# Optimization experiments

Measured on AMD Instinct MI355X. Metric: run time of the kernel, lower is better.

The kernel has to match this reference:

```python
import jax, jax.numpy as jnp
import numpy as np
from jax import lax

VTH = 0.5
GRAD_WIN = 0.5
CDECAY = 0.5
VDECAY = 0.75

@jax.custom_vjp
def pseudo_spike(v):
    # PseudoSpikeRect: heaviside fwd, rectangular surrogate grad bwd
    return (v > VTH).astype(v.dtype)

def _ps_fwd(v):
    return pseudo_spike(v), v

def _ps_bwd(v, g):
    return (g * (jnp.abs(v - VTH) < GRAD_WIN).astype(g.dtype),)

pseudo_spike.defvjp(_ps_fwd, _ps_bwd)

def conv2d(x, w, b):
    y = lax.conv_general_dilated(x, w, (1, 1), 'VALID',
                                 dimension_numbers=('NCHW', 'OIHW', 'NCHW'))
    return y + b[None, :, None, None]

def lif(psp, state):
    # CUBA-LIF: current decay + integrate, voltage decay with spike reset, threshold
    cur, volt, spk = state
    cur = CDECAY * cur + psp
    volt = VDECAY * volt * (1.0 - spk) + cur
    spk = pseudo_spike(volt)
    return spk, (cur, volt, spk)

def setup_inputs() -> dict:
    key = jax.random.key(0)
    ks = jax.random.split(key, 16)
    B, T = 64, 200
    c1, c2, c3 = 64, 128, 256
    s = lambda k, shape, scale: jax.random.normal(k, shape, jnp.float32) * scale
    return {
        'input_data': jax.random.normal(ks[0], (B, 1, 10, 10, T), jnp.float32),
        'conv1_w': s(ks[1], (c1, 1, 3, 3), 0.3), 'conv1_b': s(ks[2], (c1,), 0.1),
        'conv2_w': s(ks[3], (c2, c1, 3, 3), 0.05), 'conv2_b': s(ks[4], (c2,), 0.1),
        'conv3_w': s(ks[5], (c3, c2, 3, 3), 0.03), 'conv3_b': s(ks[6], (c3,), 0.1),
        'tc_w': s(ks[7], (3, c3, c3), 0.06), 'tc_b': s(ks[8], (3, c3), 0.1),
        'rec_w': s(ks[9], (c3, c3), 0.06), 'rec_b': s(ks[10], (c3,), 0.1),
        'fc1_w': s(ks[11], (128, c3), 0.06), 'fc1_b': s(ks[12], (128,), 0.1),
        'fc2_w': s(ks[13], (2, 128), 0.09),
        'ts_weights': jnp.ones((T, 1), jnp.float32) / T,
    }

def reference(input_data, conv1_w, conv1_b, conv2_w, conv2_b, conv3_w, conv3_b,
              tc_w, tc_b, rec_w, rec_b, fc1_w, fc1_b, fc2_w, ts_weights):
    B = input_data.shape[0]
    c1, c2, c3 = conv1_w.shape[0], conv2_w.shape[0], conv3_w.shape[0]
    f1 = fc1_w.shape[0]

    def zs(shape):
        z = jnp.zeros(shape, input_data.dtype)
        return (z, z, z)

    carry0 = (zs((B, c1, 8, 8)), zs((B, c2, 6, 6)), zs((B, c3, 1, 1)),
              zs((B, c3)), zs((B, c3)), zs((B, f1)),
              jnp.zeros((3, B, c3), input_data.dtype),  # temporal buffer, idx0 = newest
              jnp.int32(0))
    xs = jnp.moveaxis(input_data, -1, 0)  # [T, B, 1, 10, 10]

    def step_fn(carry, xw):
        c1_st, c2_st, c3_st, tc_st, r_st, f_st, buf, step = carry
        x, w = xw
        s1, c1_st = lif(conv2d(x, conv1_w, conv1_b), c1_st)       # [B,c1,8,8]
        s2, c2_st = lif(conv2d(s1, conv2_w, conv2_b), c2_st)      # [B,c2,6,6]
        p = s2.reshape(B, c2, 3, 2, 3, 2).mean(axis=(3, 5))       # AvgPool2d(2) -> [B,c2,3,3]
        s3, c3_st = lif(conv2d(p, conv3_w, conv3_b), c3_st)       # [B,c3,1,1]
        flat = s3.reshape(B, -1)                                   # [B,c3]
        buf = jnp.concatenate([flat[None], buf[:2]], axis=0)
        # temporal conv: tap i applies to spike at time t-i, only if it exists
        psp = jnp.zeros_like(flat)
        for i in range(3):
            tap = buf[i] @ tc_w[i].T + tc_b[i]
            psp = psp + jnp.where(step >= i, 1.0, 0.0).astype(tap.dtype) * tap
        s_tc, tc_st = lif(psp, tc_st)
        # recurrent cell: identity feedforward + linear on previous spike
        psp_r = s_tc + r_st[2] @ rec_w.T + rec_b
        s_r, r_st = lif(psp_r, r_st)
        s_f, f_st = lif(s_r @ fc1_w.T + fc1_b, f_st)
        out = (s_f @ fc2_w.T) * w  # w = ts_weights[step], shape [1]
        return (c1_st, c2_st, c3_st, tc_st, r_st, f_st, buf, step + 1), out

    _, outs = lax.scan(step_fn, carry0, (xs, ts_weights))
    return outs.sum(axis=0)  # [B, 2]
```

## Files before the change

kernel.cpp:

```cpp
#include <hip/hip_runtime.h>


#define B_   64
#define T_   200
#define TCB_ 50

__device__ __forceinline__ void lif32(float psp, float& cur, float& volt, float& spk) {
#pragma clang fp contract(off)
    cur  = __fadd_rn(__fmul_rn(0.5f, cur), psp);
    volt = __fadd_rn(__fmul_rn(__fmul_rn(0.75f, volt), __fsub_rn(1.0f, spk)), cur);
    spk  = (volt > 0.5f) ? 1.0f : 0.0f;
}

__global__ void k_setup(const float* __restrict__ w2, const float* __restrict__ w3,
                        const float* __restrict__ tcw, const float* __restrict__ recw,
                        const float* __restrict__ fw,
                        float* __restrict__ w2T, float* __restrict__ w3T,
                        float* __restrict__ tcT, float* __restrict__ recT,
                        float* __restrict__ fc1T) {
    int idx = blockIdx.x * 256 + threadIdx.x;
    if (idx < 73728) { int o = idx & 127, k = idx >> 7; w2T[idx] = w2[o * 576 + k]; return; }
    idx -= 73728;
    if (idx < 294912) { int o = idx & 255, k = idx >> 8; w3T[idx] = w3[o * 1152 + k]; return; }
    idx -= 294912;
    if (idx < 196608) { int tap = idx >> 16, r = idx & 65535; int o = r & 255, k = r >> 8;
                        tcT[idx] = tcw[tap * 65536 + o * 256 + k]; return; }
    idx -= 196608;
    if (idx < 65536) { int o = idx & 255, k = idx >> 8; recT[idx] = recw[o * 256 + k]; return; }
    idx -= 65536;
    if (idx < 32768) { int o = idx & 127, k = idx >> 7; fc1T[idx] = fw[o * 256 + k]; return; }
}

__global__ __launch_bounds__(256) void k_conv1(const float* __restrict__ x,
                                               const float* __restrict__ w1,
                                               const float* __restrict__ b1,
                                               unsigned char* __restrict__ s1c,
                                               float* __restrict__ st1,
                                               int t0, int TC, int first) {
    int idx = blockIdx.x * 256 + threadIdx.x;
    int xx = idx & 7, yy = (idx >> 3) & 7, o = (idx >> 6) & 63, b = idx >> 12;
    float w[9];
#pragma unroll
    for (int i = 0; i < 9; i++) w[i] = w1[o * 9 + i];
    float bias = b1[o];
    const float* xb = x + (size_t)b * 20000;
    unsigned char* sb = s1c + (size_t)b * TC * 4096 + (o << 6) + (yy << 3) + xx;
    float cur, volt, spk;
    if (first) { cur = 0.f; volt = 0.f; spk = 0.f; }
    else { cur = st1[idx]; volt = st1[262144 + idx]; spk = st1[524288 + idx]; }
    for (int tl = 0; tl < TC; tl += 4) {
        int t = t0 + tl;
        float a0 = 0.f, a1 = 0.f, a2 = 0.f, a3 = 0.f;
#pragma unroll
        for (int i = 0; i < 3; i++) {
#pragma unroll
            for (int j = 0; j < 3; j++) {
                float4 v = *(const float4*)&xb[((yy + i) * 10 + xx + j) * T_ + t];
                float wv = w[i * 3 + j];
                a0 = fmaf(wv, v.x, a0); a1 = fmaf(wv, v.y, a1);
                a2 = fmaf(wv, v.z, a2); a3 = fmaf(wv, v.w, a3);
            }
        }
        float accs[4] = {a0, a1, a2, a3};
#pragma unroll
        for (int q = 0; q < 4; q++) {
            float psp = __fadd_rn(accs[q], bias);
            lif32(psp, cur, volt, spk);
            sb[(size_t)(tl + q) * 4096] = (unsigned char)spk;
        }
    }
    st1[idx] = cur; st1[262144 + idx] = volt; st1[524288 + idx] = spk;
}

__global__ __launch_bounds__(192) void k_conv2(const unsigned char* __restrict__ s1c,
                                               const float* __restrict__ w2T,
                                               const float* __restrict__ b2,
                                               float* __restrict__ psp2c) {
    __shared__ float a_s[4096];
    int blk = blockIdx.x;
    int tid = threadIdx.x;
    const unsigned int* src4 = (const unsigned int*)(s1c + (size_t)blk * 4096);
    for (int i = tid; i < 1024; i += 192) {
        unsigned int u = src4[i];
        a_s[4 * i + 0] = (float)(u & 0xff);
        a_s[4 * i + 1] = (float)((u >> 8) & 0xff);
        a_s[4 * i + 2] = (float)((u >> 16) & 0xff);
        a_s[4 * i + 3] = (float)(u >> 24);
    }
    __syncthreads();
    int quad = tid / 6;
    int y = tid - quad * 6;
    int ob = quad << 2;
    float acc[4][6];
#pragma unroll
    for (int oo = 0; oo < 4; oo++)
#pragma unroll
        for (int xq = 0; xq < 6; xq++) acc[oo][xq] = 0.f;
    for (int c = 0; c < 64; c++) {
#pragma unroll
        for (int i = 0; i < 3; i++) {
            const float* ar = &a_s[c * 64 + (y + i) * 8];
            float4 f0 = *(const float4*)(ar);
            float4 f1 = *(const float4*)(ar + 4);
            float a[8] = {f0.x, f0.y, f0.z, f0.w, f1.x, f1.y, f1.z, f1.w};
            const float* wr = w2T + (size_t)((c * 3 + i) * 3) * 128 + ob;
#pragma unroll
            for (int j = 0; j < 3; j++) {
                float4 wv = *(const float4*)(wr + j * 128);
                float w4[4] = {wv.x, wv.y, wv.z, wv.w};
#pragma unroll
                for (int oo = 0; oo < 4; oo++)
#pragma unroll
                    for (int xq = 0; xq < 6; xq++)
                        acc[oo][xq] = fmaf(w4[oo], a[xq + j], acc[oo][xq]);
            }
        }
    }
    size_t obase = (size_t)blk * 4608 + (size_t)ob * 36 + y * 6;
#pragma unroll
    for (int oo = 0; oo < 4; oo++) {
        float bv = b2[ob + oo];
        float* dst = psp2c + obase + oo * 36;
#pragma unroll
        for (int xq = 0; xq < 6; xq++)
            dst[xq] = __fadd_rn(acc[oo][xq], bv);
    }
}

__global__ __launch_bounds__(256) void k_lif2pool(const float* __restrict__ psp2c,
                                                  float* __restrict__ pc,
                                                  float* __restrict__ st2,
                                                  int TC, int first) {
    int idx = blockIdx.x * 256 + threadIdx.x;
    int px = idx % 3; int r = idx / 3; int py = r % 3; r /= 3;
    int o = r & 127, b = r >> 7;
    const float* pb = psp2c + (size_t)b * TC * 4608 + o * 36;
    float* pd = pc + (size_t)b * TC * 1152 + o * 9 + py * 3 + px;
    int off0 = (2 * py) * 6 + 2 * px, off1 = off0 + 6;
    float c0, c1, c2, c3, v0, v1, v2, v3, s0, s1, s2, s3;
    if (first) {
        c0 = c1 = c2 = c3 = v0 = v1 = v2 = v3 = s0 = s1 = s2 = s3 = 0.f;
    } else {
        c0 = st2[idx];              c1 = st2[73728 + idx];
        c2 = st2[147456 + idx];     c3 = st2[221184 + idx];
        v0 = st2[294912 + idx];     v1 = st2[368640 + idx];
        v2 = st2[442368 + idx];     v3 = st2[516096 + idx];
        s0 = st2[589824 + idx];     s1 = st2[663552 + idx];
        s2 = st2[737280 + idx];     s3 = st2[811008 + idx];
    }
    for (int tl = 0; tl < TC; tl++) {
        const float* pt = pb + (size_t)tl * 4608;
        float2 ra = *(const float2*)(pt + off0);
        float2 rb = *(const float2*)(pt + off1);
        lif32(ra.x, c0, v0, s0);
        lif32(ra.y, c1, v1, s1);
        lif32(rb.x, c2, v2, s2);
        lif32(rb.y, c3, v3, s3);
        pd[(size_t)tl * 1152] = __fmul_rn(0.25f, __fadd_rn(__fadd_rn(__fadd_rn(s0, s1), s2), s3));
    }
    st2[idx] = c0;           st2[73728 + idx] = c1;
    st2[147456 + idx] = c2;  st2[221184 + idx] = c3;
    st2[294912 + idx] = v0;  st2[368640 + idx] = v1;
    st2[442368 + idx] = v2;  st2[516096 + idx] = v3;
    st2[589824 + idx] = s0;  st2[663552 + idx] = s1;
    st2[737280 + idx] = s2;  st2[811008 + idx] = s3;
}

__global__ __launch_bounds__(256) void k_conv3(const float* __restrict__ pc,
                                               const float* __restrict__ w3T,
                                               const float* __restrict__ b3,
                                               float* __restrict__ psp3c) {
    __shared__ float a_s[16 * 288];
    int row0 = blockIdx.x * 16;
    int tid = threadIdx.x;
    int oq = tid & 63, mg = tid >> 6;
    float acc[4][4];
#pragma unroll
    for (int oo = 0; oo < 4; oo++)
#pragma unroll
        for (int mi = 0; mi < 4; mi++) acc[oo][mi] = 0.f;
    for (int kc = 0; kc < 1152; kc += 288) {
        __syncthreads();
        for (int idx = tid; idx < 16 * 288; idx += 256) {
            int m = idx / 288, k = idx - m * 288;
            a_s[idx] = pc[(size_t)(row0 + m) * 1152 + kc + k];
        }
        __syncthreads();
        for (int k = 0; k < 288; k++) {
            float4 wv = *(const float4*)&w3T[(size_t)(kc + k) * 256 + (oq << 2)];
            float w4[4] = {wv.x, wv.y, wv.z, wv.w};
            float am[4];
#pragma unroll
            for (int mi = 0; mi < 4; mi++) am[mi] = a_s[(mg * 4 + mi) * 288 + k];
#pragma unroll
            for (int oo = 0; oo < 4; oo++)
#pragma unroll
                for (int mi = 0; mi < 4; mi++)
                    acc[oo][mi] = fmaf(w4[oo], am[mi], acc[oo][mi]);
        }
    }
#pragma unroll
    for (int mi = 0; mi < 4; mi++) {
        float* dst = psp3c + (size_t)(row0 + mg * 4 + mi) * 256 + (oq << 2);
#pragma unroll
        for (int oo = 0; oo < 4; oo++)
            dst[oo] = __fadd_rn(acc[oo][mi], b3[(oq << 2) + oo]);
    }
}

__global__ __launch_bounds__(256) void k_scan3(const float* __restrict__ psp3c,
                                               unsigned char* __restrict__ s3u8,
                                               float* __restrict__ st3,
                                               int t0, int TC, int first) {
    int idx = blockIdx.x * 256 + threadIdx.x;
    int b = idx >> 8, n = idx & 255;
    float cur, volt, spk;
    if (first) { cur = 0.f; volt = 0.f; spk = 0.f; }
    else { cur = st3[idx]; volt = st3[16384 + idx]; spk = st3[32768 + idx]; }
    for (int tl = 0; tl < TC; tl++) {
        lif32(psp3c[(size_t)(b * TC + tl) * 256 + n], cur, volt, spk);
        s3u8[((size_t)b * T_ + t0 + tl) * 256 + n] = (unsigned char)spk;
    }
    st3[idx] = cur; st3[16384 + idx] = volt; st3[32768 + idx] = spk;
}

__global__ __launch_bounds__(256) void k_tc(const unsigned char* __restrict__ s3u8,
                                            const float* __restrict__ tcT,
                                            const float* __restrict__ tc_b,
                                            float* __restrict__ ptcc, int t0) {
    __shared__ float a_s[16 * 256];
    int crow0 = blockIdx.x * 16;
    int tid = threadIdx.x;
    int oq = tid & 63, mg = tid >> 6;
    float psum[4][4];
#pragma unroll
    for (int oo = 0; oo < 4; oo++)
#pragma unroll
        for (int mi = 0; mi < 4; mi++) psum[oo][mi] = 0.f;
    for (int tap = 0; tap < 3; tap++) {
        __syncthreads();
        for (int idx = tid; idx < 16 * 256; idx += 256) {
            int m = idx >> 8, k = idx & 255;
            int crow = crow0 + m;
            int b = crow / TCB_, tl = crow - b * TCB_;
            int t = t0 + tl;
            float v = 0.f;
            if (t >= tap) v = (float)s3u8[((size_t)b * T_ + t - tap) * 256 + k];
            a_s[idx] = v;
        }
        __syncthreads();
        float acc[4][4];
#pragma unroll
        for (int oo = 0; oo < 4; oo++)
#pragma unroll
            for (int mi = 0; mi < 4; mi++) acc[oo][mi] = 0.f;
        const float* wbase = tcT + (size_t)tap * 65536 + (oq << 2);
        for (int k = 0; k < 256; k++) {
            float4 wv = *(const float4*)(wbase + (size_t)k * 256);
            float w4[4] = {wv.x, wv.y, wv.z, wv.w};
            float am[4];
#pragma unroll
            for (int mi = 0; mi < 4; mi++) am[mi] = a_s[(mg * 4 + mi) * 256 + k];
#pragma unroll
            for (int oo = 0; oo < 4; oo++)
#pragma unroll
                for (int mi = 0; mi < 4; mi++)
                    acc[oo][mi] = fmaf(w4[oo], am[mi], acc[oo][mi]);
        }
#pragma unroll
        for (int mi = 0; mi < 4; mi++) {
            int crow = crow0 + mg * 4 + mi;
            int b = crow / TCB_, tl = crow - b * TCB_;
            int t = t0 + tl;
            float g = (t >= tap) ? 1.0f : 0.0f;
#pragma unroll
            for (int oo = 0; oo < 4; oo++) {
                int oc = (oq << 2) + oo;
                float tap_f = __fadd_rn(acc[oo][mi], tc_b[tap * 256 + oc]);
                psum[oo][mi] = __fadd_rn(psum[oo][mi], __fmul_rn(g, tap_f));
            }
        }
    }
#pragma unroll
    for (int mi = 0; mi < 4; mi++) {
        int crow = crow0 + mg * 4 + mi;
        float* dst = ptcc + (size_t)crow * 256 + (oq << 2);
#pragma unroll
        for (int oo = 0; oo < 4; oo++) dst[oo] = psum[oo][mi];
    }
}

__global__ __launch_bounds__(256) void k_scan_tc(const float* __restrict__ ptcc,
                                                 unsigned char* __restrict__ s_tc8,
                                                 float* __restrict__ st_tc,
                                                 int t0, int first) {
    int idx = blockIdx.x * 256 + threadIdx.x;
    int b = idx >> 8, n = idx & 255;
    float cur, volt, spk;
    if (first) { cur = 0.f; volt = 0.f; spk = 0.f; }
    else { cur = st_tc[idx]; volt = st_tc[16384 + idx]; spk = st_tc[32768 + idx]; }
    for (int tl = 0; tl < TCB_; tl++) {
        lif32(ptcc[(size_t)(b * TCB_ + tl) * 256 + n], cur, volt, spk);
        s_tc8[((size_t)b * T_ + t0 + tl) * 256 + n] = (unsigned char)spk;
    }
    st_tc[idx] = cur; st_tc[16384 + idx] = volt; st_tc[32768 + idx] = spk;
}

__global__ __launch_bounds__(512, 1) void k_rec(const unsigned char* __restrict__ s_tc8,
                                                const float* __restrict__ rec_w,
                                                const float* __restrict__ rec_b,
                                                unsigned char* __restrict__ s_r8) {
    __shared__ __align__(16) float spk_s[2][256];
    __shared__ float acc_s[256];
    int b = blockIdx.x;
    int tid = threadIdx.x;
    int o = tid & 255, half = tid >> 8;
    float w[128];
#pragma unroll
    for (int j = 0; j < 32; j++) {
        float4 v = *(const float4*)&rec_w[(size_t)o * 256 + (half << 7) + 4 * j];
        w[4 * j + 0] = v.x; w[4 * j + 1] = v.y;
        w[4 * j + 2] = v.z; w[4 * j + 3] = v.w;
    }
#pragma unroll
    for (int k = 0; k < 128; k++) asm volatile("" : "+v"(w[k]));
    if (half == 0) spk_s[0][o] = 0.f;
    float cur = 0.f, volt = 0.f, spk = 0.f;
    float rb = rec_b[o];
    const unsigned char* stp = s_tc8 + (size_t)b * T_ * 256 + o;
    unsigned char* srp = s_r8 + (size_t)b * T_ * 256 + o;
    __syncthreads();
    int p = 0;
    for (int t = 0; t < T_; t++) {
        if (half == 0) {
            const float* sp = spk_s[p];
            float acc = 0.f;
#pragma unroll
            for (int k = 0; k < 128; k += 4) {
                float4 sv = *(const float4*)&sp[k];
                acc = fmaf(sv.x, w[k + 0], acc);
                acc = fmaf(sv.y, w[k + 1], acc);
                acc = fmaf(sv.z, w[k + 2], acc);
                acc = fmaf(sv.w, w[k + 3], acc);
            }
            acc_s[o] = acc;
        }
        __syncthreads();
        if (half == 1) {
            float stc = (float)stp[(size_t)t * 256];
            const float* sp = spk_s[p] + 128;
            float acc = acc_s[o];
#pragma unroll
            for (int k = 0; k < 128; k += 4) {
                float4 sv = *(const float4*)&sp[k];
                acc = fmaf(sv.x, w[k + 0], acc);
                acc = fmaf(sv.y, w[k + 1], acc);
                acc = fmaf(sv.z, w[k + 2], acc);
                acc = fmaf(sv.w, w[k + 3], acc);
            }
            float psp = __fadd_rn(__fadd_rn(stc, acc), rb);
            lif32(psp, cur, volt, spk);
            srp[(size_t)t * 256] = (unsigned char)spk;
            spk_s[p ^ 1][o] = spk;
        }
        __syncthreads();
        p ^= 1;
    }
}

__global__ __launch_bounds__(256) void k_fc1(const unsigned char* __restrict__ s_r8,
                                             const float* __restrict__ fc1T,
                                             const float* __restrict__ fc1_b,
                                             float* __restrict__ pfc, int t0) {
    __shared__ float a_s[16 * 256];
    int crow0 = blockIdx.x * 16;
    int tid = threadIdx.x;
    int oq = tid & 31, mg = tid >> 5;
    float acc[4][2];
#pragma unroll
    for (int oo = 0; oo < 4; oo++) { acc[oo][0] = 0.f; acc[oo][1] = 0.f; }
    for (int idx = tid; idx < 16 * 256; idx += 256) {
        int m = idx >> 8, k = idx & 255;
        int crow = crow0 + m;
        int b = crow / TCB_, tl = crow - b * TCB_;
        a_s[idx] = (float)s_r8[((size_t)b * T_ + t0 + tl) * 256 + k];
    }
    __syncthreads();
    for (int k = 0; k < 256; k++) {
        float4 wv = *(const float4*)&fc1T[(size_t)k * 128 + (oq << 2)];
        float w4[4] = {wv.x, wv.y, wv.z, wv.w};
        float a0 = a_s[(mg * 2 + 0) * 256 + k];
        float a1 = a_s[(mg * 2 + 1) * 256 + k];
#pragma unroll
        for (int oo = 0; oo < 4; oo++) {
            acc[oo][0] = fmaf(w4[oo], a0, acc[oo][0]);
            acc[oo][1] = fmaf(w4[oo], a1, acc[oo][1]);
        }
    }
#pragma unroll
    for (int mi = 0; mi < 2; mi++) {
        float* dst = pfc + (size_t)(crow0 + mg * 2 + mi) * 128 + (oq << 2);
#pragma unroll
        for (int oo = 0; oo < 4; oo++)
            dst[oo] = __fadd_rn(acc[oo][mi], fc1_b[(oq << 2) + oo]);
    }
}

__global__ __launch_bounds__(256) void k_scan_f(const float* __restrict__ pfc,
                                                unsigned char* __restrict__ s_f8,
                                                float* __restrict__ st_f,
                                                int t0, int first) {
    int idx = blockIdx.x * 256 + threadIdx.x;
    int b = idx >> 7, n = idx & 127;
    float cur, volt, spk;
    if (first) { cur = 0.f; volt = 0.f; spk = 0.f; }
    else { cur = st_f[idx]; volt = st_f[8192 + idx]; spk = st_f[16384 + idx]; }
    for (int tl = 0; tl < TCB_; tl++) {
        lif32(pfc[(size_t)(b * TCB_ + tl) * 128 + n], cur, volt, spk);
        s_f8[((size_t)b * T_ + t0 + tl) * 128 + n] = (unsigned char)spk;
    }
    st_f[idx] = cur; st_f[8192 + idx] = volt; st_f[16384 + idx] = spk;
}

__global__ __launch_bounds__(128) void k_final(const unsigned char* __restrict__ s_f8,
                                               const float* __restrict__ ts,
                                               const float* __restrict__ fc2,
                                               float* __restrict__ out) {
    __shared__ double q_s[128];
    int b = blockIdx.x, k = threadIdx.x;
    double q = 0.0;
    const unsigned char* sf = s_f8 + (size_t)b * T_ * 128 + k;
    for (int t = 0; t < T_; t++) q = fma((double)ts[t], (double)sf[(size_t)t * 128], q);
    q_s[k] = q;
    __syncthreads();
    if (k < 2) {
        double o = 0.0;
        for (int kk = 0; kk < 128; kk++) o = fma((double)fc2[k * 128 + kk], q_s[kk], o);
        out[b * 2 + k] = (float)o;
    }
}

extern "C" void kernel_launch(void* const* d_in, const int* in_sizes, int n_in,
                              void* d_out, int out_size, void* d_ws, size_t ws_size,
                              hipStream_t stream) {
    const float* x       = (const float*)d_in[0];
    const float* conv1_w = (const float*)d_in[1];
    const float* conv1_b = (const float*)d_in[2];
    const float* conv2_w = (const float*)d_in[3];
    const float* conv2_b = (const float*)d_in[4];
    const float* conv3_w = (const float*)d_in[5];
    const float* conv3_b = (const float*)d_in[6];
    const float* tc_w    = (const float*)d_in[7];
    const float* tc_b    = (const float*)d_in[8];
    const float* rec_w   = (const float*)d_in[9];
    const float* rec_b   = (const float*)d_in[10];
    const float* fc1_w   = (const float*)d_in[11];
    const float* fc1_b   = (const float*)d_in[12];
    const float* fc2_w   = (const float*)d_in[13];
    const float* ts_w    = (const float*)d_in[14];
    float* out = (float*)d_out;
    (void)in_sizes; (void)n_in; (void)out_size;

    char* base = (char*)d_ws;
    float* w2T  = (float*)(base + 0);
    float* w3T  = (float*)(base + 294912);
    float* tcT  = (float*)(base + 1474560);
    float* recT = (float*)(base + 2260992);
    float* fc1T = (float*)(base + 2523136);
    float* st1  = (float*)(base + 2654208);
    float* st2  = (float*)(base + 5799936);
    float* st3  = (float*)(base + 9338880);
    float* st_tc= (float*)(base + 9535488);
    float* st_f = (float*)(base + 9732096);
    unsigned char* s3u8  = (unsigned char*)(base + 9830400);
    unsigned char* s_tc8 = (unsigned char*)(base + 13107200);
    unsigned char* s_r8  = (unsigned char*)(base + 16384000);
    unsigned char* s_f8  = (unsigned char*)(base + 19660800);

    const size_t PERS = 21299200;
    const size_t PER_T = 1802240;
    int TCF;
    if      (ws_size >= PERS + 40 * PER_T) TCF = 40;
    else if (ws_size >= PERS + 20 * PER_T) TCF = 20;
    else if (ws_size >= PERS +  8 * PER_T) TCF = 8;
    else                                   TCF = 4;
    int NCH = T_ / TCF;
    char* cb = base + PERS;
    float* psp2c = (float*)(cb);
    float* psp3c = (float*)(cb + (size_t)TCF * 1179648);
    float* pc    = (float*)(cb + (size_t)TCF * (1179648 + 65536));
    unsigned char* s1c = (unsigned char*)(cb + (size_t)TCF * (1179648 + 65536 + 294912));
    float* ptcc = (float*)(cb);
    float* pfc  = (float*)(cb + 3276800);

    k_setup<<<2592, 256, 0, stream>>>(conv2_w, conv3_w, tc_w, rec_w, fc1_w,
                                      w2T, w3T, tcT, recT, fc1T);
    for (int ch = 0; ch < NCH; ch++) {
        int t0 = ch * TCF;
        int first = (ch == 0) ? 1 : 0;
        k_conv1<<<1024, 256, 0, stream>>>(x, conv1_w, conv1_b, s1c, st1, t0, TCF, first);
        k_conv2<<<B_ * TCF, 192, 0, stream>>>(s1c, w2T, conv2_b, psp2c);
        k_lif2pool<<<288, 256, 0, stream>>>(psp2c, pc, st2, TCF, first);
        k_conv3<<<B_ * TCF / 16, 256, 0, stream>>>(pc, w3T, conv3_b, psp3c);
        k_scan3<<<64, 256, 0, stream>>>(psp3c, s3u8, st3, t0, TCF, first);
    }
    for (int bc = 0; bc < T_ / TCB_; bc++) {
        int t0 = bc * TCB_;
        k_tc<<<B_ * TCB_ / 16, 256, 0, stream>>>(s3u8, tcT, tc_b, ptcc, t0);
        k_scan_tc<<<64, 256, 0, stream>>>(ptcc, s_tc8, st_tc, t0, (bc == 0) ? 1 : 0);
    }
    k_rec<<<64, 512, 0, stream>>>(s_tc8, rec_w, rec_b, s_r8);
    for (int bc = 0; bc < T_ / TCB_; bc++) {
        int t0 = bc * TCB_;
        k_fc1<<<B_ * TCB_ / 16, 256, 0, stream>>>(s_r8, fc1T, fc1_b, pfc, t0);
        k_scan_f<<<32, 256, 0, stream>>>(pfc, s_f8, st_f, t0, (bc == 0) ? 1 : 0);
    }
    k_final<<<64, 128, 0, stream>>>(s_f8, ts_w, fc2_w, out);
}
```

Measured before the change: 2.474 ms.

## Fuse conv2 with LIF and avg-pool, re-tile conv3 with fewer rows per block

Conv2 is fused with the layer-2 LIF scan and 2x2 average pooling. Each block handles one batch item and 16 output channels, keeps those channels' weights in shared memory, and loops over time inside the kernel. This removes the large psp2c intermediate buffer and one kernel launch per chunk, and shrinks the per-timestep workspace. Conv3 now loads 4 full rows into shared memory and computes 4 outputs per thread instead of 16. That gives up register reuse of the weight loads in exchange for more blocks. The fused conv2 keeps only 144 of 192 threads active and runs just 512 blocks, with per-timestep syncs, so its parallelism is lower.

```diff
diff --git a/kernel.cpp b/kernel.cpp
--- a/kernel.cpp
+++ b/kernel.cpp
@@ -72,140 +72,121 @@
     st1[idx] = cur; st1[262144 + idx] = volt; st1[524288 + idx] = spk;
 }
 
-__global__ __launch_bounds__(192) void k_conv2(const unsigned char* __restrict__ s1c,
-                                               const float* __restrict__ w2T,
-                                               const float* __restrict__ b2,
-                                               float* __restrict__ psp2c) {
-    __shared__ float a_s[4096];
+__global__ __launch_bounds__(192) void k_conv2f(const unsigned char* __restrict__ s1c,
+                                                const float* __restrict__ w2,
+                                                const float* __restrict__ b2,
+                                                float* __restrict__ pc,
+                                                float* __restrict__ st2,
+                                                int TC, int first) {
+    __shared__ float w_s[16 * 576];
+    __shared__ float s_s[4096];
     int blk = blockIdx.x;
+    int b = blk >> 3, og = blk & 7;
     int tid = threadIdx.x;
-    const unsigned int* src4 = (const unsigned int*)(s1c + (size_t)blk * 4096);
-    for (int i = tid; i < 1024; i += 192) {
-        unsigned int u = src4[i];
-        a_s[4 * i + 0] = (float)(u & 0xff);
-        a_s[4 * i + 1] = (float)((u >> 8) & 0xff);
-        a_s[4 * i + 2] = (float)((u >> 16) & 0xff);
-        a_s[4 * i + 3] = (float)(u >> 24);
-    }
-    __syncthreads();
-    int quad = tid / 6;
-    int y = tid - quad * 6;
-    int ob = quad << 2;
-    float acc[4][6];
-#pragma unroll
-    for (int oo = 0; oo < 4; oo++)
-#pragma unroll
-        for (int xq = 0; xq < 6; xq++) acc[oo][xq] = 0.f;
-    for (int c = 0; c < 64; c++) {
-#pragma unroll
-        for (int i = 0; i < 3; i++) {
-            const float* ar = &a_s[c * 64 + (y + i) * 8];
-            float4 f0 = *(const float4*)(ar);
-            float4 f1 = *(const float4*)(ar + 4);
-            float a[8] = {f0.x, f0.y, f0.z, f0.w, f1.x, f1.y, f1.z, f1.w};
-            const float* wr = w2T + (size_t)((c * 3 + i) * 3) * 128 + ob;
-#pragma unroll
-            for (int j = 0; j < 3; j++) {
-                float4 wv = *(const float4*)(wr + j * 128);
-                float w4[4] = {wv.x, wv.y, wv.z, wv.w};
-#pragma unroll
-                for (int oo = 0; oo < 4; oo++)
-#pragma unroll
-                    for (int xq = 0; xq < 6; xq++)
-                        acc[oo][xq] = fmaf(w4[oo], a[xq + j], acc[oo][xq]);
-            }
-        }
-    }
-    size_t obase = (size_t)blk * 4608 + (size_t)ob * 36 + y * 6;
-#pragma unroll
-    for (int oo = 0; oo < 4; oo++) {
-        float bv = b2[ob + oo];
-        float* dst = psp2c + obase + oo * 36;
-#pragma unroll
-        for (int xq = 0; xq < 6; xq++)
-            dst[xq] = __fadd_rn(acc[oo][xq], bv);
-    }
-}
-
-__global__ __launch_bounds__(256) void k_lif2pool(const float* __restrict__ psp2c,
-                                                  float* __restrict__ pc,
-                                                  float* __restrict__ st2,
-                                                  int TC, int first) {
-    int idx = blockIdx.x * 256 + threadIdx.x;
-    int px = idx % 3; int r = idx / 3; int py = r % 3; r /= 3;
-    int o = r & 127, b = r >> 7;
-    const float* pb = psp2c + (size_t)b * TC * 4608 + o * 36;
-    float* pd = pc + (size_t)b * TC * 1152 + o * 9 + py * 3 + px;
-    int off0 = (2 * py) * 6 + 2 * px, off1 = off0 + 6;
-    float c0, c1, c2, c3, v0, v1, v2, v3, s0, s1, s2, s3;
-    if (first) {
-        c0 = c1 = c2 = c3 = v0 = v1 = v2 = v3 = s0 = s1 = s2 = s3 = 0.f;
-    } else {
-        c0 = st2[idx];              c1 = st2[73728 + idx];
-        c2 = st2[147456 + idx];     c3 = st2[221184 + idx];
-        v0 = st2[294912 + idx];     v1 = st2[368640 + idx];
-        v2 = st2[442368 + idx];     v3 = st2[516096 + idx];
-        s0 = st2[589824 + idx];     s1 = st2[663552 + idx];
-        s2 = st2[737280 + idx];     s3 = st2[811008 + idx];
-    }
+    for (int i = tid; i < 9216; i += 192) w_s[i] = w2[(size_t)og * 9216 + i];
+    bool act = tid < 144;
+    int ol = tid / 9, pos = tid - ol * 9;
+    int py = pos / 3, px = pos - py * 3;
+    int oc = (og << 4) + ol;
+    int sidx = act ? ((b * 128 + oc) * 9 + pos) : 0;
+    float cur[4], volt[4], spk[4];
+#pragma unroll
+    for (int q = 0; q < 4; q++) { cur[q] = 0.f; volt[q] = 0.f; spk[q] = 0.f; }
+    if (act && !first) {
+#pragma unroll
+        for (int q = 0; q < 4; q++) {
+            cur[q]  = st2[(size_t)q * 73728 + sidx];
+            volt[q] = st2[(size_t)(4 + q) * 73728 + sidx];
+            spk[q]  = st2[(size_t)(8 + q) * 73728 + sidx];
+        }
+    }
+    float bias = act ? b2[oc] : 0.f;
+    const float* ws = &w_s[ol * 576];
     for (int tl = 0; tl < TC; tl++) {
-        const float* pt = pb + (size_t)tl * 4608;
-        float2 ra = *(const float2*)(pt + off0);
-        float2 rb = *(const float2*)(pt + off1);
-        lif32(ra.x, c0, v0, s0);
-        lif32(ra.y, c1, v1, s1);
-        lif32(rb.x, c2, v2, s2);
-        lif32(rb.y, c3, v3, s3);
-        pd[(size_t)tl * 1152] = __fmul_rn(0.25f, __fadd_rn(__fadd_rn(__fadd_rn(s0, s1), s2), s3));
-    }
-    st2[idx] = c0;           st2[73728 + idx] = c1;
-    st2[147456 + idx] = c2;  st2[221184 + idx] = c3;
-    st2[294912 + idx] = v0;  st2[368640 + idx] = v1;
-    st2[442368 + idx] = v2;  st2[516096 + idx] = v3;
-    st2[589824 + idx] = s0;  st2[663552 + idx] = s1;
-    st2[737280 + idx] = s2;  st2[811008 + idx] = s3;
+        __syncthreads();
+        const unsigned int* src4 = (const unsigned int*)(s1c + (size_t)(b * TC + tl) * 4096);
+        for (int i = tid; i < 1024; i += 192) {
+            unsigned int u = src4[i];
+            s_s[4 * i + 0] = (float)(u & 0xff);
+            s_s[4 * i + 1] = (float)((u >> 8) & 0xff);
+            s_s[4 * i + 2] = (float)((u >> 16) & 0xff);
+            s_s[4 * i + 3] = (float)(u >> 24);
+        }
+        __syncthreads();
+        if (act) {
+            float a0 = 0.f, a1 = 0.f, a2 = 0.f, a3 = 0.f;
+            for (int c = 0; c < 64; c++) {
+                const float* sc = &s_s[c * 64];
+                float win[4][4];
+#pragma unroll
+                for (int dy = 0; dy < 4; dy++) {
+                    const float* r = &sc[(2 * py + dy) * 8 + 2 * px];
+                    float2 u0 = *(const float2*)r;
+                    float2 u1 = *(const float2*)(r + 2);
+                    win[dy][0] = u0.x; win[dy][1] = u0.y;
+                    win[dy][2] = u1.x; win[dy][3] = u1.y;
+                }
+                const float* wc = ws + c * 9;
+#pragma unroll
+                for (int i = 0; i < 3; i++)
+#pragma unroll
+                    for (int j = 0; j < 3; j++) {
+                        float w = wc[i * 3 + j];
+                        a0 = fmaf(w, win[i][j],         a0);
+                        a1 = fmaf(w, win[i][j + 1],     a1);
+                        a2 = fmaf(w, win[i + 1][j],     a2);
+                        a3 = fmaf(w, win[i + 1][j + 1], a3);
+                    }
+            }
+            float accq[4] = {a0, a1, a2, a3};
+#pragma unroll
+            for (int q = 0; q < 4; q++) {
+                float psp = __fadd_rn(accq[q], bias);
+                lif32(psp, cur[q], volt[q], spk[q]);
+            }
+            float pool = __fmul_rn(0.25f,
+                __fadd_rn(__fadd_rn(__fadd_rn(spk[0], spk[1]), spk[2]), spk[3]));
+            pc[(size_t)(b * TC + tl) * 1152 + oc * 9 + pos] = pool;
+        }
+    }
+    if (act) {
+#pragma unroll
+        for (int q = 0; q < 4; q++) {
+            st2[(size_t)q * 73728 + sidx]       = cur[q];
+            st2[(size_t)(4 + q) * 73728 + sidx] = volt[q];
+            st2[(size_t)(8 + q) * 73728 + sidx] = spk[q];
+        }
+    }
 }
 
 __global__ __launch_bounds__(256) void k_conv3(const float* __restrict__ pc,
                                                const float* __restrict__ w3T,
                                                const float* __restrict__ b3,
                                                float* __restrict__ psp3c) {
-    __shared__ float a_s[16 * 288];
-    int row0 = blockIdx.x * 16;
+    __shared__ float a_s[4 * 1152];
+    int row0 = blockIdx.x * 4;
     int tid = threadIdx.x;
     int oq = tid & 63, mg = tid >> 6;
-    float acc[4][4];
+    for (int idx = tid; idx < 4 * 1152; idx += 256) {
+        int m = idx / 1152, k = idx - m * 1152;
+        a_s[idx] = pc[(size_t)(row0 + m) * 1152 + k];
+    }
+    __syncthreads();
+    float acc[4] = {0.f, 0.f, 0.f, 0.f};
+    const float* as_row = &a_s[mg * 1152];
+#pragma unroll 4
+    for (int k = 0; k < 1152; k++) {
+        float4 wv = *(const float4*)&w3T[(size_t)k * 256 + (oq << 2)];
+        float am = as_row[k];
+        acc[0] = fmaf(wv.x, am, acc[0]);
+        acc[1] = fmaf(wv.y, am, acc[1]);
+        acc[2] = fmaf(wv.z, am, acc[2]);
+        acc[3] = fmaf(wv.w, am, acc[3]);
+    }
+    float* dst = psp3c + (size_t)(row0 + mg) * 256 + (oq << 2);
 #pragma unroll
     for (int oo = 0; oo < 4; oo++)
-#pragma unroll
-        for (int mi = 0; mi < 4; mi++) acc[oo][mi] = 0.f;
-    for (int kc = 0; kc < 1152; kc += 288) {
-        __syncthreads();
-        for (int idx = tid; idx < 16 * 288; idx += 256) {
-            int m = idx / 288, k = idx - m * 288;
-            a_s[idx] = pc[(size_t)(row0 + m) * 1152 + kc + k];
-        }
-        __syncthreads();
-        for (int k = 0; k < 288; k++) {
-            float4 wv = *(const float4*)&w3T[(size_t)(kc + k) * 256 + (oq << 2)];
-            float w4[4] = {wv.x, wv.y, wv.z, wv.w};
-            float am[4];
-#pragma unroll
-            for (int mi = 0; mi < 4; mi++) am[mi] = a_s[(mg * 4 + mi) * 288 + k];
-#pragma unroll
-            for (int oo = 0; oo < 4; oo++)
-#pragma unroll
-                for (int mi = 0; mi < 4; mi++)
-                    acc[oo][mi] = fmaf(w4[oo], am[mi], acc[oo][mi]);
-        }
-    }
-#pragma unroll
-    for (int mi = 0; mi < 4; mi++) {
-        float* dst = psp3c + (size_t)(row0 + mg * 4 + mi) * 256 + (oq << 2);
-#pragma unroll
-        for (int oo = 0; oo < 4; oo++)
-            dst[oo] = __fadd_rn(acc[oo][mi], b3[(oq << 2) + oo]);
-    }
+        dst[oo] = __fadd_rn(acc[oo], b3[(oq << 2) + oo]);
 }
 
 __global__ __launch_bounds__(256) void k_scan3(const float* __restrict__ psp3c,
@@ -478,18 +459,16 @@
     unsigned char* s_f8  = (unsigned char*)(base + 19660800);
 
     const size_t PERS = 21299200;
-    const size_t PER_T = 1802240;
+    const size_t PER_T = 622592;
     int TCF;
     if      (ws_size >= PERS + 40 * PER_T) TCF = 40;
     else if (ws_size >= PERS + 20 * PER_T) TCF = 20;
-    else if (ws_size >= PERS +  8 * PER_T) TCF = 8;
-    else                                   TCF = 4;
+    else                                   TCF = 8;
     int NCH = T_ / TCF;
     char* cb = base + PERS;
-    float* psp2c = (float*)(cb);
-    float* psp3c = (float*)(cb + (size_t)TCF * 1179648);
-    float* pc    = (float*)(cb + (size_t)TCF * (1179648 + 65536));
-    unsigned char* s1c = (unsigned char*)(cb + (size_t)TCF * (1179648 + 65536 + 294912));
+    float* psp3c = (float*)(cb);
+    float* pc    = (float*)(cb + (size_t)TCF * 65536);
+    unsigned char* s1c = (unsigned char*)(cb + (size_t)TCF * (65536 + 294912));
     float* ptcc = (float*)(cb);
     float* pfc  = (float*)(cb + 3276800);
 
@@ -499,9 +478,8 @@
         int t0 = ch * TCF;
         int first = (ch == 0) ? 1 : 0;
         k_conv1<<<1024, 256, 0, stream>>>(x, conv1_w, conv1_b, s1c, st1, t0, TCF, first);
-        k_conv2<<<B_ * TCF, 192, 0, stream>>>(s1c, w2T, conv2_b, psp2c);
-        k_lif2pool<<<288, 256, 0, stream>>>(psp2c, pc, st2, TCF, first);
-        k_conv3<<<B_ * TCF / 16, 256, 0, stream>>>(pc, w3T, conv3_b, psp3c);
+        k_conv2f<<<512, 192, 0, stream>>>(s1c, conv2_w, conv2_b, pc, st2, TCF, first);
+        k_conv3<<<B_ * TCF / 4, 256, 0, stream>>>(pc, w3T, conv3_b, psp3c);
         k_scan3<<<64, 256, 0, stream>>>(psp3c, s3u8, st3, t0, TCF, first);
     }
     for (int bc = 0; bc < T_ / TCB_; bc++) {
```

Result: slower. 5.662 ms (+128.8%).
